# Kernel optimization log

Measured on AMD Instinct MI355X. Metric: run time of the kernel, lower is better.

The kernel has to match this reference:

```python
import jax, jax.numpy as jnp
import numpy as np

CS = [32, 32, 64, 128, 256, 256, 128, 96, 96]
NC = 19
N0, N1, N2, N3, N4 = 50000, 20000, 8000, 3200, 1300


def build_shapes():
    cs = CS
    def rb(ci, co):
        t = [(27, ci, co), (27, co, co)]
        if ci != co:
            t.append((ci, co))  # 1x1 shortcut conv
        return t
    s = [(27, 4, cs[0]), (27, cs[0], cs[0])]                       # stem
    s += [(8, cs[0], cs[0])] + rb(cs[0], cs[1]) + rb(cs[1], cs[1])  # stage1
    s += [(8, cs[1], cs[1])] + rb(cs[1], cs[2]) + rb(cs[2], cs[2])  # stage2
    s += [(8, cs[2], cs[2])] + rb(cs[2], cs[3]) + rb(cs[3], cs[3])  # stage3
    s += [(8, cs[3], cs[3])] + rb(cs[3], cs[4]) + rb(cs[4], cs[4])  # stage4
    s += [(8, cs[4], cs[5])] + rb(cs[5] + cs[3], cs[5]) + rb(cs[5], cs[5])  # up1
    s += [(8, cs[5], cs[6])] + rb(cs[6] + cs[2], cs[6]) + rb(cs[6], cs[6])  # up2
    s += [(8, cs[6], cs[7])] + rb(cs[7] + cs[1], cs[7]) + rb(cs[7], cs[7])  # up3
    s += [(8, cs[7], cs[8])] + rb(cs[8] + cs[0], cs[8]) + rb(cs[8], cs[8])  # up4
    s += [(cs[8], NC), (NC,), (cs[8], cs[8]), (cs[8],), (cs[8], 128), (128,)]
    return s

P_TOTAL = sum(int(np.prod(sh)) for sh in build_shapes())


def _bn(x):
    # train-mode BatchNorm, gamma=1 beta=0 (set by weight_initialization)
    return (x - x.mean(0)) * jax.lax.rsqrt(jnp.var(x, 0) + 1e-5)


def _spconv(x, nbr, W):
    # sparse conv as gather-GEMM-scatter over K kernel offsets.
    # x: [Nin, Cin], nbr: [Nout, K] row indices into x, W: [K, Cin, Cout]
    acc0 = jnp.zeros((nbr.shape[0], W.shape[-1]), x.dtype)
    def step(acc, kw):
        idx, Wk = kw
        return acc + x[idx] @ Wk, None
    acc, _ = jax.lax.scan(step, acc0, (nbr.T, W))
    return acc


def _spdeconv(x, parent, off, W):
    # transposed ks=2 stride=2 conv: each fine voxel has exactly one coarse
    # parent and one kernel-offset id. out[i] = x[parent[i]] @ W[off[i]]
    y = jnp.einsum('nc,kcd->nkd', x[parent], W)  # [Nf, 8, Cout]
    return jnp.take_along_axis(y, off[:, None, None], axis=1)[:, 0, :]


def _cbr(x, nbr, W):
    return jax.nn.relu(_bn(_spconv(x, nbr, W)))


def _resblock(x, nbr, take, ci, co):
    w1 = take(); w2 = take()
    h = _bn(_spconv(jax.nn.relu(_bn(_spconv(x, nbr, w1))), nbr, w2))
    s = x if ci == co else _bn(x @ take())
    return jax.nn.relu(h + s)


def _forward(x, nbr0, nbr1, nbr2, nbr3, nbr4, d1, d2, d3, d4,
             u1p, u1o, u2p, u2o, u3p, u3o, u4p, u4o, params):
    parts = []
    o = 0
    for sh in build_shapes():
        n = int(np.prod(sh))
        parts.append(params[o:o + n].reshape(sh))
        o += n
    it = iter(parts)
    take = lambda: next(it)
    cs = CS
    x0 = _cbr(x, nbr0, take()); x0 = _cbr(x0, nbr0, take())            # stem
    h = _cbr(x0, d1, take())
    h = _resblock(h, nbr1, take, cs[0], cs[1]); x1 = _resblock(h, nbr1, take, cs[1], cs[1])
    h = _cbr(x1, d2, take())
    h = _resblock(h, nbr2, take, cs[1], cs[2]); x2 = _resblock(h, nbr2, take, cs[2], cs[2])
    h = _cbr(x2, d3, take())
    h = _resblock(h, nbr3, take, cs[2], cs[3]); x3 = _resblock(h, nbr3, take, cs[3], cs[3])
    h = _cbr(x3, d4, take())
    h = _resblock(h, nbr4, take, cs[3], cs[4]); x4 = _resblock(h, nbr4, take, cs[4], cs[4])
    y = jax.nn.relu(_bn(_spdeconv(x4, u1p, u1o, take())))
    y = jnp.concatenate([y, x3], 1)
    y = _resblock(y, nbr3, take, cs[5] + cs[3], cs[5]); y = _resblock(y, nbr3, take, cs[5], cs[5])
    y = jax.nn.relu(_bn(_spdeconv(y, u2p, u2o, take())))
    y = jnp.concatenate([y, x2], 1)
    y = _resblock(y, nbr2, take, cs[6] + cs[2], cs[6]); y = _resblock(y, nbr2, take, cs[6], cs[6])
    y = jax.nn.relu(_bn(_spdeconv(y, u3p, u3o, take())))
    y = jnp.concatenate([y, x1], 1)
    y = _resblock(y, nbr1, take, cs[7] + cs[1], cs[7]); y = _resblock(y, nbr1, take, cs[7], cs[7])
    y = jax.nn.relu(_bn(_spdeconv(y, u4p, u4o, take())))
    y = jnp.concatenate([y, x0], 1)
    y = _resblock(y, nbr0, take, cs[8] + cs[0], cs[8]); y = _resblock(y, nbr0, take, cs[8], cs[8])
    wc = take(); bc = take(); w1 = take(); b1 = take(); w2 = take(); b2 = take()
    out = y @ wc + bc                             # classifier logits [N0, NC]
    feat = jax.nn.relu(y @ w1 + b1) @ w2 + b2     # projection head [N0, 128]
    return out, feat


def setup_inputs() -> dict:
    key = jax.random.key(0)
    ks = jax.random.split(key, 20)
    ri = lambda k, shape, hi: jax.random.randint(k, shape, 0, hi, dtype=jnp.int32)
    return {
        'x': jax.random.normal(ks[0], (N0, 4), jnp.float32),
        'nbr0': ri(ks[1], (N0, 27), N0), 'nbr1': ri(ks[2], (N1, 27), N1),
        'nbr2': ri(ks[3], (N2, 27), N2), 'nbr3': ri(ks[4], (N3, 27), N3),
        'nbr4': ri(ks[5], (N4, 27), N4),
        'd1': ri(ks[6], (N1, 8), N0), 'd2': ri(ks[7], (N2, 8), N1),
        'd3': ri(ks[8], (N3, 8), N2), 'd4': ri(ks[9], (N4, 8), N3),
        'u1p': ri(ks[10], (N3,), N4), 'u1o': ri(ks[11], (N3,), 8),
        'u2p': ri(ks[12], (N2,), N3), 'u2o': ri(ks[13], (N2,), 8),
        'u3p': ri(ks[14], (N1,), N2), 'u3o': ri(ks[15], (N1,), 8),
        'u4p': ri(ks[16], (N0,), N1), 'u4o': ri(ks[17], (N0,), 8),
        'params': jax.random.normal(ks[18], (P_TOTAL,), jnp.float32) * 0.05,
    }


def reference(x, nbr0, nbr1, nbr2, nbr3, nbr4, d1, d2, d3, d4,
              u1p, u1o, u2p, u2o, u3p, u3o, u4p, u4o, params):
    return _forward(x, nbr0, nbr1, nbr2, nbr3, nbr4, d1, d2, d3, d4,
                    u1p, u1o, u2p, u2o, u3p, u3o, u4p, u4o, params)
```

## Files before the change

kernel.cpp:

```cpp
#include <hip/hip_runtime.h>
#include <hip/hip_bf16.h>
#include <stdint.h>

typedef __hip_bfloat16 hbf;
typedef unsigned short u16;
typedef __attribute__((ext_vector_type(8))) short bfrag;
typedef _Float16 __attribute__((ext_vector_type(8))) hfrag;
typedef __attribute__((ext_vector_type(4))) float f4;

#define NP0 50000
#define NP1 20000
#define NP2 8000
#define NP3 3200
#define NP4 1300

static inline int cdiv(int a, int b) { return (a + b - 1) / b; }

static __device__ __forceinline__ float u2f(u16 u) { return __uint_as_float(((unsigned)u) << 16); }
static __device__ __forceinline__ u16 f2u(float f) {
  hbf h = __float2bfloat16(f);
  u16 r; __builtin_memcpy(&r, &h, 2); return r;
}
static __device__ __forceinline__ u16 f2h(float f) {
  _Float16 h = (_Float16)f;
  u16 r; __builtin_memcpy(&r, &h, 2); return r;
}
static __device__ __forceinline__ float h2f(u16 u) {
  _Float16 h; __builtin_memcpy(&h, &u, 2); return (float)h;
}
static __device__ __forceinline__ float pload(const void* P, int isbf, size_t i) {
  return isbf ? u2f(((const u16*)P)[i]) : ((const float*)P)[i];
}


struct PrepD {
  long cpre, src, dst;
  int K, CI, CO, CB32, NT16, hf;
};

__global__ void k_sniff(const void* __restrict__ xraw, int* __restrict__ flagp) {
  __shared__ float smax[256];
  const u16* u = (const u16*)xraw;
  float m = 0.f;
  for (int i = threadIdx.x; i < 2048; i += 256) {
    float v = u2f(u[2 * i]);
    if (isnan(v) || isinf(v)) m = 1e30f; else m = fmaxf(m, fabsf(v));
  }
  smax[threadIdx.x] = m;
  __syncthreads();
  for (int s = 128; s > 0; s >>= 1) {
    if (threadIdx.x < s) smax[threadIdx.x] = fmaxf(smax[threadIdx.x], smax[threadIdx.x + s]);
    __syncthreads();
  }
  if (threadIdx.x == 0) *flagp = (smax[0] < 1e4f) ? 1 : 0;
}

__global__ __launch_bounds__(256) void k_prep_all(
    const void* __restrict__ P, const int* __restrict__ flagp, u16* __restrict__ W,
    const PrepD* __restrict__ T, int NL, long totalC, long totalE)
{
  int f = *flagp;
  int L = 0;
  for (long c = (long)blockIdx.x * 256 + threadIdx.x; c < totalC; c += (long)gridDim.x * 256) {
    while (L + 1 < NL && c >= T[L + 1].cpre) ++L;
    PrepD d = T[L];
    long lc = c - d.cpre;
    int lane = (int)(lc & 63); long t = lc >> 6;
    int nt = (int)(t % d.NT16); t /= d.NT16;
    int cb = (int)(t % d.CB32); int k = (int)(t / d.CB32);
    int co = nt * 16 + (lane & 15);
    int cib = cb * 32 + (lane >> 4) * 8;
    u16 hi[8], lo[8];
#pragma unroll
    for (int j = 0; j < 8; ++j) {
      int ci = cib + j; float v = 0.f;
      if (ci < d.CI && co < d.CO) v = pload(P, f, d.src + ((size_t)k * d.CI + ci) * d.CO + co);
      if (d.hf) { u16 h = f2h(v); hi[j] = h; lo[j] = f2h(v - h2f(h)); }
      else      { u16 h = f2u(v); hi[j] = h; lo[j] = f2u(v - u2f(h)); }
    }
    *(bfrag*)(W + d.dst + lc * 8) = *(const bfrag*)hi;
    *(bfrag*)(W + totalE + d.dst + lc * 8) = *(const bfrag*)lo;
  }
}

__global__ __launch_bounds__(256) void k_prep_frag(
    const void* __restrict__ P, const int* __restrict__ flagp, u16* __restrict__ W,
    long src, long halfel, int hf, int K, int CI, int CO, int CB32, int NT16)
{
  int f = *flagp;
  long total = (long)K * CB32 * NT16 * 64;
  for (long c = (long)blockIdx.x * 256 + threadIdx.x; c < total; c += (long)gridDim.x * 256) {
    int lane = (int)(c & 63); long t = c >> 6;
    int nt = (int)(t % NT16); t /= NT16;
    int cb = (int)(t % CB32); int k = (int)(t / CB32);
    int co = nt * 16 + (lane & 15);
    int cib = cb * 32 + (lane >> 4) * 8;
    u16 hi[8], lo[8];
#pragma unroll
    for (int j = 0; j < 8; ++j) {
      int ci = cib + j; float v = 0.f;
      if (ci < CI && co < CO) v = pload(P, f, src + ((size_t)k * CI + ci) * CO + co);
      if (hf) { u16 h = f2h(v); hi[j] = h; lo[j] = f2h(v - h2f(h)); }
      else    { u16 h = f2u(v); hi[j] = h; lo[j] = f2u(v - u2f(h)); }
    }
    *(bfrag*)(W + c * 8) = *(const bfrag*)hi;
    *(bfrag*)(W + halfel + c * 8) = *(const bfrag*)lo;
  }
}

__global__ void k_prep_bias(const void* __restrict__ P, const int* __restrict__ flagp,
                            float* __restrict__ B, long src, int n)
{
  int f = *flagp;
  int i = blockIdx.x * 256 + threadIdx.x;
  if (i < n) B[i] = pload(P, f, src + i);
}

__global__ void k_pad(const void* __restrict__ xraw, const int* __restrict__ flagp,
                      float* __restrict__ Xp, int N)
{
  int f = *flagp; int total = N * 32;
  for (int i = blockIdx.x * 256 + threadIdx.x; i < total; i += gridDim.x * 256) {
    int n = i >> 5, cc = i & 31;
    Xp[i] = (cc < 4) ? pload(xraw, f, (size_t)n * 4 + cc) : 0.f;
  }
}

template<int NT>
__global__ __launch_bounds__(256) void k_conv_mfma(
    const void* __restrict__ Xv, const int* __restrict__ nbr,
    const u16* __restrict__ Wp, long halfel, float* __restrict__ Y,
    const float* __restrict__ bias, int relu, const int* __restrict__ flagp,
    int ahalf, int N, int K, int CB32, int NT16, int CO, int XS, int tlen, int atomic)
{
  const int f = *flagp;
  const int lane = threadIdx.x & 63;
  const int wv = threadIdx.x >> 6;
  const int rowbase = blockIdx.x * 128 + wv * 32;
  const int ntb = blockIdx.y * NT;
  const int ml = lane & 15;
  const int quad = lane >> 4;
  const int ktot = K * CB32;
  const int t0 = blockIdx.z * tlen;
  const int t1 = (t0 + tlen < ktot) ? (t0 + tlen) : ktot;
  if (t0 >= t1) return;

  f4 acc[2][NT];
#pragma unroll
  for (int i = 0; i < 2; ++i)
#pragma unroll
    for (int j = 0; j < NT; ++j) acc[i][j] = (f4)(0.f);

  int k = t0 / CB32;
  int cb = t0 - k * CB32;
  int idx[2];
  bool fresh = true;

  if (ahalf) {
    const u16* X = (const u16*)Xv;
    if (f) {
      for (int t = t0; t < t1; ++t) {
        if (fresh) {
#pragma unroll
          for (int mt = 0; mt < 2; ++mt) {
            int r = rowbase + mt * 16 + ml;
            idx[mt] = (r < N) ? (nbr ? nbr[(size_t)r * K + k] : r) : 0;
          }
          fresh = false;
        }
        const u16* WH = Wp + (size_t)t * NT16 * 512;
        hfrag bh[NT];
#pragma unroll
        for (int nt = 0; nt < NT; ++nt)
          bh[nt] = *(const hfrag*)(WH + ((size_t)(ntb + nt) * 64 + lane) * 8);
        hfrag a[2];
#pragma unroll
        for (int mt = 0; mt < 2; ++mt)
          a[mt] = *(const hfrag*)(X + (size_t)idx[mt] * XS + cb * 32 + quad * 8);
#pragma unroll
        for (int mt = 0; mt < 2; ++mt)
#pragma unroll
          for (int nt = 0; nt < NT; ++nt)
            acc[mt][nt] = __builtin_amdgcn_mfma_f32_16x16x32_f16(a[mt], bh[nt], acc[mt][nt], 0, 0, 0);
        if (++cb == CB32) { cb = 0; ++k; fresh = true; }
      }
    } else {
      for (int t = t0; t < t1; ++t) {
        if (fresh) {
#pragma unroll
          for (int mt = 0; mt < 2; ++mt) {
            int r = rowbase + mt * 16 + ml;
            idx[mt] = (r < N) ? (nbr ? nbr[(size_t)r * K + k] : r) : 0;
          }
          fresh = false;
        }
        const u16* WH = Wp + (size_t)t * NT16 * 512;
        const u16* WL = WH + halfel;
        hfrag bh[NT], bl[NT];
#pragma unroll
        for (int nt = 0; nt < NT; ++nt) {
          size_t o = ((size_t)(ntb + nt) * 64 + lane) * 8;
          bh[nt] = *(const hfrag*)(WH + o);
          bl[nt] = *(const hfrag*)(WL + o);
        }
        hfrag a[2];
#pragma unroll
        for (int mt = 0; mt < 2; ++mt)
          a[mt] = *(const hfrag*)(X + (size_t)idx[mt] * XS + cb * 32 + quad * 8);
#pragma unroll
        for (int mt = 0; mt < 2; ++mt)
#pragma unroll
          for (int nt = 0; nt < NT; ++nt) {
            acc[mt][nt] = __builtin_amdgcn_mfma_f32_16x16x32_f16(a[mt], bl[nt], acc[mt][nt], 0, 0, 0);
            acc[mt][nt] = __builtin_amdgcn_mfma_f32_16x16x32_f16(a[mt], bh[nt], acc[mt][nt], 0, 0, 0);
          }
        if (++cb == CB32) { cb = 0; ++k; fresh = true; }
      }
    }
  } else {
    const float* X = (const float*)Xv;
    if (f) {
      for (int t = t0; t < t1; ++t) {
        if (fresh) {
#pragma unroll
          for (int mt = 0; mt < 2; ++mt) {
            int r = rowbase + mt * 16 + ml;
            idx[mt] = (r < N) ? (nbr ? nbr[(size_t)r * K + k] : r) : 0;
          }
          fresh = false;
        }
        const u16* WH = Wp + (size_t)t * NT16 * 512;
        bfrag bh[NT];
#pragma unroll
        for (int nt = 0; nt < NT; ++nt)
          bh[nt] = *(const bfrag*)(WH + ((size_t)(ntb + nt) * 64 + lane) * 8);
        bfrag ahi[2], alo[2];
#pragma unroll
        for (int mt = 0; mt < 2; ++mt) {
          const float* ap = X + (size_t)idx[mt] * XS + cb * 32 + quad * 8;
          float4 q0 = *(const float4*)ap;
          float4 q1 = *(const float4*)(ap + 4);
          float av[8] = {q0.x, q0.y, q0.z, q0.w, q1.x, q1.y, q1.z, q1.w};
          u16 hi8[8], lo8[8];
#pragma unroll
          for (int j = 0; j < 8; ++j) {
            u16 hh = f2u(av[j]);
            hi8[j] = hh;
            lo8[j] = f2u(av[j] - u2f(hh));
          }
          __builtin_memcpy(&ahi[mt], hi8, 16);
          __builtin_memcpy(&alo[mt], lo8, 16);
        }
#pragma unroll
        for (int mt = 0; mt < 2; ++mt)
#pragma unroll
          for (int nt = 0; nt < NT; ++nt) {
            acc[mt][nt] = __builtin_amdgcn_mfma_f32_16x16x32_bf16(alo[mt], bh[nt], acc[mt][nt], 0, 0, 0);
            acc[mt][nt] = __builtin_amdgcn_mfma_f32_16x16x32_bf16(ahi[mt], bh[nt], acc[mt][nt], 0, 0, 0);
          }
        if (++cb == CB32) { cb = 0; ++k; fresh = true; }
      }
    } else {
      for (int t = t0; t < t1; ++t) {
        if (fresh) {
#pragma unroll
          for (int mt = 0; mt < 2; ++mt) {
            int r = rowbase + mt * 16 + ml;
            idx[mt] = (r < N) ? (nbr ? nbr[(size_t)r * K + k] : r) : 0;
          }
          fresh = false;
        }
        const u16* WH = Wp + (size_t)t * NT16 * 512;
        const u16* WL = WH + halfel;
        bfrag bh[NT], bl[NT];
#pragma unroll
        for (int nt = 0; nt < NT; ++nt) {
          size_t o = ((size_t)(ntb + nt) * 64 + lane) * 8;
          bh[nt] = *(const bfrag*)(WH + o);
          bl[nt] = *(const bfrag*)(WL + o);
        }
        bfrag ahi[2], alo[2];
#pragma unroll
        for (int mt = 0; mt < 2; ++mt) {
          const float* ap = X + (size_t)idx[mt] * XS + cb * 32 + quad * 8;
          float4 q0 = *(const float4*)ap;
          float4 q1 = *(const float4*)(ap + 4);
          float av[8] = {q0.x, q0.y, q0.z, q0.w, q1.x, q1.y, q1.z, q1.w};
          u16 hi8[8], lo8[8];
#pragma unroll
          for (int j = 0; j < 8; ++j) {
            u16 hh = f2u(av[j]);
            hi8[j] = hh;
            lo8[j] = f2u(av[j] - u2f(hh));
          }
          __builtin_memcpy(&ahi[mt], hi8, 16);
          __builtin_memcpy(&alo[mt], lo8, 16);
        }
#pragma unroll
        for (int mt = 0; mt < 2; ++mt)
#pragma unroll
          for (int nt = 0; nt < NT; ++nt) {
            acc[mt][nt] = __builtin_amdgcn_mfma_f32_16x16x32_bf16(alo[mt], bh[nt], acc[mt][nt], 0, 0, 0);
            acc[mt][nt] = __builtin_amdgcn_mfma_f32_16x16x32_bf16(ahi[mt], bl[nt], acc[mt][nt], 0, 0, 0);
            acc[mt][nt] = __builtin_amdgcn_mfma_f32_16x16x32_bf16(ahi[mt], bh[nt], acc[mt][nt], 0, 0, 0);
          }
        if (++cb == CB32) { cb = 0; ++k; fresh = true; }
      }
    }
  }

#pragma unroll
  for (int mt = 0; mt < 2; ++mt) {
#pragma unroll
    for (int nt = 0; nt < NT; ++nt) {
      int col = (ntb + nt) * 16 + ml;
      if (col >= CO) continue;
      float bvv = bias ? bias[col] : 0.f;
#pragma unroll
      for (int reg = 0; reg < 4; ++reg) {
        int row = rowbase + mt * 16 + quad * 4 + reg;
        if (row < N) {
          if (atomic) {
            atomicAdd(&Y[(size_t)row * CO + col], acc[mt][nt][reg]);
          } else {
            float v = acc[mt][nt][reg] + bvv;
            if (relu) v = fmaxf(v, 0.f);
            Y[(size_t)row * CO + col] = v;
          }
        }
      }
    }
  }
}

__global__ void k_bias_relu(float* __restrict__ Y, const float* __restrict__ bias,
                            u16* __restrict__ d16, int relu, int total, int CO)
{
  int stride = gridDim.x * 256;
  for (int i = blockIdx.x * 256 + threadIdx.x; i < total; i += stride) {
    int c = i % CO;
    float v = Y[i] + (bias ? bias[c] : 0.f);
    if (relu) v = fmaxf(v, 0.f);
    Y[i] = v;
    if (d16) d16[i] = f2h(v);
  }
}

static void launch_conv(hipStream_t s, int bx, const void* X, const int* nbr,
                        const u16* W, long halfel, float* Y, const float* bias, int relu,
                        const int* flagp, int ahalf, int N, int K, int CB32, int NT16, int CO, int XS,
                        u16* d16)
{
  int NT = (NT16 % 6 == 0) ? 6 : ((NT16 % 4 == 0) ? 4 : 2);
  int ny = NT16 / NT;
  int ktot = K * CB32;
  long blocks = (long)bx * ny;
  int ZS = 1;
  if (ktot > 1) {
    ZS = (int)((1024 + blocks - 1) / blocks);
    if (ZS > ktot) ZS = ktot;
    if (ZS < 1) ZS = 1;
  }
  int tlen = cdiv(ktot, ZS);
  ZS = cdiv(ktot, tlen);
  int atomic = (ZS > 1) ? 1 : 0;
  if (atomic) hipMemsetAsync(Y, 0, (size_t)N * CO * 4, s);
  dim3 g(bx, ny, ZS);
  if (NT == 6)      k_conv_mfma<6><<<g, 256, 0, s>>>(X, nbr, W, halfel, Y, bias, relu, flagp, ahalf, N, K, CB32, NT16, CO, XS, tlen, atomic);
  else if (NT == 4) k_conv_mfma<4><<<g, 256, 0, s>>>(X, nbr, W, halfel, Y, bias, relu, flagp, ahalf, N, K, CB32, NT16, CO, XS, tlen, atomic);
  else              k_conv_mfma<2><<<g, 256, 0, s>>>(X, nbr, W, halfel, Y, bias, relu, flagp, ahalf, N, K, CB32, NT16, CO, XS, tlen, atomic);
  if ((atomic && (bias || relu)) || d16) {
    int total = N * CO;
    int nb = cdiv(total, 1024); if (nb > 1024) nb = 1024; if (nb < 1) nb = 1;
    k_bias_relu<<<nb, 256, 0, s>>>(Y, atomic ? bias : nullptr, d16, atomic ? relu : 0, total, CO);
  }
}

__global__ __launch_bounds__(256) void k_deconv(
    const void* __restrict__ Xv, const int* __restrict__ par, const int* __restrict__ off,
    const void* __restrict__ P, long wofs, const int* __restrict__ flagp,
    float* __restrict__ Y, int xmode, int N, int CI, int CO)
{
  int f = *flagp;
  int lane = threadIdx.x & 63, wv = threadIdx.x >> 6;
  int n = blockIdx.y * 4 + wv; if (n >= N) return;
  int co = blockIdx.x * 64 + lane; if (co >= CO) return;
  size_t wbase = wofs + (size_t)off[n] * CI * CO + co;
  float acc = 0.f;
  if (xmode) {
    const u16* xr = (const u16*)Xv + (size_t)par[n] * CI;
    for (int ci = 0; ci < CI; ci += 4) {
      ushort4 xv = *(const ushort4*)(xr + ci);
      acc += h2f(xv.x) * pload(P, f, wbase + (size_t)ci * CO);
      acc += h2f(xv.y) * pload(P, f, wbase + (size_t)(ci + 1) * CO);
      acc += h2f(xv.z) * pload(P, f, wbase + (size_t)(ci + 2) * CO);
      acc += h2f(xv.w) * pload(P, f, wbase + (size_t)(ci + 3) * CO);
    }
  } else {
    const float* xr = (const float*)Xv + (size_t)par[n] * CI;
    for (int ci = 0; ci < CI; ci += 4) {
      float4 xv = *(const float4*)(xr + ci);
      acc += xv.x * pload(P, f, wbase + (size_t)ci * CO);
      acc += xv.y * pload(P, f, wbase + (size_t)(ci + 1) * CO);
      acc += xv.z * pload(P, f, wbase + (size_t)(ci + 2) * CO);
      acc += xv.w * pload(P, f, wbase + (size_t)(ci + 3) * CO);
    }
  }
  Y[(size_t)n * CO + co] = acc;
}

__global__ __launch_bounds__(256) void k_bn_stats(
    const float* __restrict__ X, float* __restrict__ st, int total, int C)
{
  __shared__ float ssum[384], ssq[384];
  for (int c = threadIdx.x; c < C; c += 256) { ssum[c] = 0.f; ssq[c] = 0.f; }
  __syncthreads();
  int gid = blockIdx.x * 256 + threadIdx.x;
  int total4 = total >> 2;
  int stride = gridDim.x * 256;
  int c0 = (gid * 4) % C;
  float s0 = 0.f, s1 = 0.f, s2 = 0.f, s3 = 0.f;
  float q0 = 0.f, q1 = 0.f, q2 = 0.f, q3 = 0.f;
  for (int i = gid; i < total4; i += stride) {
    float4 v = ((const float4*)X)[i];
    s0 += v.x; q0 += v.x * v.x;
    s1 += v.y; q1 += v.y * v.y;
    s2 += v.z; q2 += v.z * v.z;
    s3 += v.w; q3 += v.w * v.w;
  }
  atomicAdd(&ssum[c0], s0);     atomicAdd(&ssq[c0], q0);
  atomicAdd(&ssum[c0 + 1], s1); atomicAdd(&ssq[c0 + 1], q1);
  atomicAdd(&ssum[c0 + 2], s2); atomicAdd(&ssq[c0 + 2], q2);
  atomicAdd(&ssum[c0 + 3], s3); atomicAdd(&ssq[c0 + 3], q3);
  __syncthreads();
  for (int c = threadIdx.x; c < C; c += 256) {
    atomicAdd(&st[c], ssum[c]); atomicAdd(&st[384 + c], ssq[c]);
  }
}

__global__ __launch_bounds__(256) void k_bn_apply(
    const float* __restrict__ X, const float* __restrict__ st,
    const void* __restrict__ addp, int addmode,
    void* __restrict__ Yo, int outmode, int relu, int total, int C, float invN)
{
  __shared__ float mean[384], rsig[384];
  for (int c = threadIdx.x; c < C; c += 256) {
    float mm = st[c] * invN;
    float vv = st[384 + c] * invN - mm * mm;
    mean[c] = mm; rsig[c] = rsqrtf(vv + 1e-5f);
  }
  __syncthreads();
  int gid = blockIdx.x * 256 + threadIdx.x;
  int total4 = total >> 2;
  int stride = gridDim.x * 256;
  int c0 = (gid * 4) % C;
  float m0 = mean[c0], m1 = mean[c0 + 1], m2 = mean[c0 + 2], m3 = mean[c0 + 3];
  float r0 = rsig[c0], r1 = rsig[c0 + 1], r2 = rsig[c0 + 2], r3 = rsig[c0 + 3];
  for (int i = gid; i < total4; i += stride) {
    float4 v = ((const float4*)X)[i];
    float w0 = (v.x - m0) * r0, w1 = (v.y - m1) * r1;
    float w2 = (v.z - m2) * r2, w3 = (v.w - m3) * r3;
    if (addmode == 1) {
      float4 a = ((const float4*)addp)[i];
      w0 += a.x; w1 += a.y; w2 += a.z; w3 += a.w;
    } else if (addmode == 2) {
      ushort4 ah = *(const ushort4*)((const u16*)addp + (size_t)i * 4);
      w0 += h2f(ah.x); w1 += h2f(ah.y); w2 += h2f(ah.z); w3 += h2f(ah.w);
    }
    if (relu) {
      w0 = fmaxf(w0, 0.f); w1 = fmaxf(w1, 0.f);
      w2 = fmaxf(w2, 0.f); w3 = fmaxf(w3, 0.f);
    }
    if (outmode == 0) {
      float4 o; o.x = w0; o.y = w1; o.z = w2; o.w = w3;
      ((float4*)Yo)[i] = o;
    } else {
      ushort4 hh; hh.x = f2h(w0); hh.y = f2h(w1); hh.z = f2h(w2); hh.w = f2h(w3);
      *(ushort4*)((u16*)Yo + (size_t)i * 4) = hh;
    }
  }
}

__global__ void k_copycols(const void* __restrict__ Sv, u16* __restrict__ D,
                           int smode, int N, int Cs, int Cd, int off)
{
  int csq = Cs >> 2;
  int total4 = N * csq;
  int stride = gridDim.x * 256;
  for (int i = blockIdx.x * 256 + threadIdx.x; i < total4; i += stride) {
    int n = i / csq, cc = (i - n * csq) * 4;
    ushort4 hh;
    if (smode == 0) {
      float4 v = ((const float4*)Sv)[i];
      hh.x = f2h(v.x); hh.y = f2h(v.y); hh.z = f2h(v.z); hh.w = f2h(v.w);
    } else {
      hh = *(const ushort4*)((const u16*)Sv + (size_t)i * 4);
    }
    *(ushort4*)(D + (size_t)n * Cd + off + cc) = hh;
  }
}

__global__ void k_store_dyn(const float* __restrict__ S, void* __restrict__ D,
                            const int* __restrict__ flagp, size_t eofs, int n)
{
  int f = *flagp;
  int n4 = n >> 2;
  int stride = gridDim.x * 256;
  for (int i = blockIdx.x * 256 + threadIdx.x; i < n4; i += stride) {
    float4 v = ((const float4*)S)[i];
    if (f) {
      ushort4 u;
      u.x = f2u(v.x); u.y = f2u(v.y); u.z = f2u(v.z); u.w = f2u(v.w);
      *(ushort4*)((u16*)D + eofs + (size_t)i * 4) = u;
    } else {
      *(float4*)((float*)D + eofs + (size_t)i * 4) = v;
    }
  }
}

static int build_table(PrepD* T, long* totalC, long* totalE) {
  int n = 0; long po = 0, ce = 0, cc = 0;
  auto W = [&](int K, int CI, int CO, int hf) {
    int CB = cdiv(CI, 32), NTx = cdiv(CO, 16);
    long ch = (long)K * CB * NTx * 64;
    T[n].cpre = cc; T[n].src = po; T[n].dst = ce;
    T[n].K = K; T[n].CI = CI; T[n].CO = CO; T[n].CB32 = CB; T[n].NT16 = NTx; T[n].hf = hf;
    ++n; cc += ch; ce += ch * 8; po += (long)K * CI * CO;
  };
  auto SKIP = [&](long e) { po += e; };
  W(27, 4, 32, 0); W(27, 32, 32, 0);
  W(8, 32, 32, 0); W(27, 32, 32, 0); W(27, 32, 32, 0); W(27, 32, 32, 0); W(27, 32, 32, 0);
  W(8, 32, 32, 0); W(27, 32, 64, 0); W(27, 64, 64, 0); W(1, 32, 64, 0); W(27, 64, 64, 0); W(27, 64, 64, 0);
  W(8, 64, 64, 0); W(27, 64, 128, 0); W(27, 128, 128, 0); W(1, 64, 128, 0); W(27, 128, 128, 0); W(27, 128, 128, 0);
  W(8, 128, 128, 0); W(27, 128, 256, 0); W(27, 256, 256, 0); W(1, 128, 256, 0); W(27, 256, 256, 0); W(27, 256, 256, 0);
  SKIP(8L * 256 * 256);
  W(27, 384, 256, 1); W(27, 256, 256, 1); W(1, 384, 256, 1); W(27, 256, 256, 1); W(27, 256, 256, 1);
  SKIP(8L * 256 * 128);
  W(27, 192, 128, 1); W(27, 128, 128, 1); W(1, 192, 128, 1); W(27, 128, 128, 1); W(27, 128, 128, 1);
  SKIP(8L * 128 * 96);
  W(27, 128, 96, 1); W(27, 96, 96, 1); W(1, 128, 96, 1); W(27, 96, 96, 1); W(27, 96, 96, 1);
  SKIP(8L * 96 * 96);
  W(27, 128, 96, 1); W(27, 96, 96, 1); W(1, 128, 96, 1); W(27, 96, 96, 1); W(27, 96, 96, 1);
  W(1, 96, 19, 1); SKIP(19); W(1, 96, 96, 1); SKIP(96); W(1, 96, 128, 1); SKIP(128);
  *totalC = cc; *totalE = ce;
  return n;
}

extern "C" void kernel_launch(void* const* d_in, const int* in_sizes, int n_in,
                              void* d_out, int out_size, void* d_ws, size_t ws_size,
                              hipStream_t stream)
{
  const void* xraw = d_in[0];
  const int* nbr0 = (const int*)d_in[1];
  const int* nbr1 = (const int*)d_in[2];
  const int* nbr2 = (const int*)d_in[3];
  const int* nbr3 = (const int*)d_in[4];
  const int* nbr4 = (const int*)d_in[5];
  const int* d1 = (const int*)d_in[6];
  const int* d2 = (const int*)d_in[7];
  const int* d3 = (const int*)d_in[8];
  const int* d4 = (const int*)d_in[9];
  const int* u1p = (const int*)d_in[10]; const int* u1o = (const int*)d_in[11];
  const int* u2p = (const int*)d_in[12]; const int* u2o = (const int*)d_in[13];
  const int* u3p = (const int*)d_in[14]; const int* u3o = (const int*)d_in[15];
  const int* u4p = (const int*)d_in[16]; const int* u4o = (const int*)d_in[17];
  const void* params = d_in[18];
  (void)in_sizes; (void)n_in;

  static PrepD h_table[64];
  long totalC = 0, totalE = 0;
  int NL = build_table(h_table, &totalC, &totalE);

  char* base = (char*)d_ws; size_t off = 0;
  auto ab = [&](size_t bytes) -> void* { void* p = base + off; off += (bytes + 63) & ~(size_t)63; return p; };
  int* flagp = (int*)ab(64);
  float* st = (float*)ab((size_t)64 * 768 * 4);
  float* Bstf = (float*)ab((size_t)512 * 4);
  float* x0 = (float*)ab((size_t)NP0 * 32 * 4);
  float* x1 = (float*)ab((size_t)NP1 * 32 * 4);
  float* x2 = (float*)ab((size_t)NP2 * 64 * 4);
  float* x3 = (float*)ab((size_t)NP3 * 128 * 4);
  float* x4 = (float*)ab((size_t)NP4 * 256 * 4);
  float* U  = (float*)ab((size_t)NP0 * 96 * 4);
  float* A  = (float*)ab((size_t)NP0 * 96 * 4);
  float* B  = (float*)ab((size_t)NP0 * 128 * 4);
  float* Xp = B;

  size_t wall_bytes = (size_t)totalE * 4;
  size_t rem = (ws_size > off) ? (ws_size - off) : 0;
  bool bigprep = rem >= wall_bytes + 8192;
  u16* Wall = nullptr; PrepD* d_table = nullptr; u16* Wst = nullptr;
  if (bigprep) {
    Wall = (u16*)ab(wall_bytes);
    d_table = (PrepD*)ab(4096);
  } else {
    Wst = (u16*)ab((size_t)5400000 * 2);
  }
  if (off > ws_size) { hipMemsetAsync(d_out, 0, (size_t)out_size * 2, stream); return; }

  long po = 0;
  int bnc = 0;
  int wli = 0;

  auto prepF = [&](int hf, int K, int CI, int CO, int CB32, int NT16) -> long {
    long chunks = (long)K * CB32 * NT16 * 64;
    long halfel = chunks * 8;
    int nb = (int)((chunks + 255) / 256); if (nb > 4096) nb = 4096; if (nb < 1) nb = 1;
    k_prep_frag<<<nb, 256, 0, stream>>>(params, flagp, Wst, po, halfel, hf, K, CI, CO, CB32, NT16);
    po += (long)K * CI * CO;
    return halfel;
  };
  auto getW = [&](int hf, int K, int CI, int CO, int CB32, int NT16, const u16** Wp, long* he) {
    if (bigprep) {
      *Wp = Wall + h_table[wli].dst; *he = totalE;
      ++wli; po += (long)K * CI * CO;
    } else {
      *he = prepF(hf, K, CI, CO, CB32, NT16); *Wp = Wst;
    }
  };
  auto convop = [&](int hf, const void* X, const int* nb_, int K, int CI, int CO, float* Y, int N, int XS) {
    int CB32 = cdiv(CI, 32), NT16 = cdiv(CO, 16);
    const u16* Wp; long he;
    getW(hf, K, CI, CO, CB32, NT16, &Wp, &he);
    launch_conv(stream, cdiv(N, 128), X, nb_, Wp, he, Y, nullptr, 0, flagp, hf, N, K, CB32, NT16, CO, XS, nullptr);
  };
  auto linop = [&](int hf, const void* X, int CI, int CO, float* Y, int N, bool bias, int relu, u16* d16) {
    int CB32 = cdiv(CI, 32), NT16 = cdiv(CO, 16);
    const u16* Wp; long he;
    getW(hf, 1, CI, CO, CB32, NT16, &Wp, &he);
    const float* bp = nullptr;
    if (bias) {
      k_prep_bias<<<cdiv(CO, 256), 256, 0, stream>>>(params, flagp, Bstf, po, CO);
      po += CO; bp = Bstf;
    }
    launch_conv(stream, cdiv(N, 128), X, nullptr, Wp, he, Y, bp, relu, flagp, hf, N, 1, CB32, NT16, CO, CI, d16);
  };
  auto deconvop = [&](const void* X, int xmode, const int* par, const int* ofv, int CI, int CO, float* Y, int N) {
    long wofs = po; po += (long)8 * CI * CO;
    dim3 g(cdiv(CO, 64), cdiv(N, 4));
    k_deconv<<<g, 256, 0, stream>>>(X, par, ofv, params, wofs, flagp, Y, xmode, N, CI, CO);
  };
  auto bnop = [&](const float* X, int N, int C, const void* addp, int addmode, int relu,
                  void* out, int outmode) {
    float* slot = st + (size_t)(bnc++) * 768;
    int total = N * C;
    int total4 = total >> 2;
    int nb1 = cdiv(total4, 4096); if (nb1 > 504) nb1 = 504; if (nb1 < 3) nb1 = 3;
    nb1 = ((nb1 + 2) / 3) * 3;
    k_bn_stats<<<nb1, 256, 0, stream>>>(X, slot, total, C);
    int nb2 = cdiv(total4, 2048); if (nb2 > 510) nb2 = 510; if (nb2 < 3) nb2 = 3;
    nb2 = ((nb2 + 2) / 3) * 3;
    k_bn_apply<<<nb2, 256, 0, stream>>>(X, slot, addp, addmode, out ? out : (void*)X, outmode,
                                        relu, total, C, 1.0f / (float)N);
  };
  auto copyop = [&](const void* S, int smode, u16* D, int N, int Cs, int Cd, int o2) {
    int total4 = (N * Cs) >> 2;
    int nb3 = cdiv(total4, 1024); if (nb3 > 1024) nb3 = 1024; if (nb3 < 1) nb3 = 1;
    k_copycols<<<nb3, 256, 0, stream>>>(S, D, smode, N, Cs, Cd, o2);
  };
  auto storeop = [&](const float* S, size_t eo, int n) {
    int nb4 = cdiv(n >> 2, 1024); if (nb4 > 1024) nb4 = 1024; if (nb4 < 1) nb4 = 1;
    k_store_dyn<<<nb4, 256, 0, stream>>>(S, d_out, flagp, eo, n);
  };
  auto resblock = [&](const int* nb, int N, int CI, int CO,
                      float* H, float* t1, float* t2, float* OUT) {
    convop(0, H, nb, 27, CI, CO, t1, N, CI);
    bnop(t1, N, CO, nullptr, 0, 1, nullptr, 0);
    convop(0, t1, nb, 27, CO, CO, t2, N, CO);
    const float* S;
    if (CI == CO) S = H;
    else { linop(0, H, CI, CO, t1, N, false, 0, nullptr); bnop(t1, N, CO, nullptr, 0, 0, nullptr, 0); S = t1; }
    bnop(t2, N, CO, S, 1, 1, OUT, 0);
  };
  auto resblock16 = [&](const int* nb, int N, int CI, int CO,
                        u16* H16, float* t1, float* t2, u16* OUT16) {
    convop(1, H16, nb, 27, CI, CO, t1, N, CI);
    bnop(t1, N, CO, nullptr, 0, 1, (u16*)t2, 1);
    convop(1, (u16*)t2, nb, 27, CO, CO, t1, N, CO);
    if (CI == CO) {
      bnop(t1, N, CO, H16, 2, 1, OUT16, 1);
    } else {
      linop(1, H16, CI, CO, t2, N, false, 0, nullptr);
      bnop(t2, N, CO, nullptr, 0, 0, OUT16, 1);
      bnop(t1, N, CO, OUT16, 2, 1, OUT16, 1);
    }
  };

  k_sniff<<<1, 256, 0, stream>>>(xraw, flagp);
  if (bigprep) {
    hipMemcpyAsync(d_table, h_table, (size_t)NL * sizeof(PrepD), hipMemcpyHostToDevice, stream);
    int nbp = (int)((totalC + 255) / 256); if (nbp > 4096) nbp = 4096;
    k_prep_all<<<nbp, 256, 0, stream>>>(params, flagp, Wall, d_table, NL, totalC, totalE);
  }
  hipMemsetAsync(st, 0, (size_t)64 * 768 * 4, stream);
  k_pad<<<1024, 256, 0, stream>>>(xraw, flagp, Xp, NP0);

  convop(0, Xp, nbr0, 27, 4, 32, A, NP0, 32);  bnop(A, NP0, 32, nullptr, 0, 1, nullptr, 0);
  convop(0, A, nbr0, 27, 32, 32, x0, NP0, 32); bnop(x0, NP0, 32, nullptr, 0, 1, nullptr, 0);
  convop(0, x0, d1, 8, 32, 32, U, NP1, 32); bnop(U, NP1, 32, nullptr, 0, 1, nullptr, 0);
  resblock(nbr1, NP1, 32, 32, U, A, B, U);
  resblock(nbr1, NP1, 32, 32, U, A, B, x1);
  convop(0, x1, d2, 8, 32, 32, U, NP2, 32); bnop(U, NP2, 32, nullptr, 0, 1, nullptr, 0);
  resblock(nbr2, NP2, 32, 64, U, A, B, U);
  resblock(nbr2, NP2, 64, 64, U, A, B, x2);
  convop(0, x2, d3, 8, 64, 64, U, NP3, 64); bnop(U, NP3, 64, nullptr, 0, 1, nullptr, 0);
  resblock(nbr3, NP3, 64, 128, U, A, B, U);
  resblock(nbr3, NP3, 128, 128, U, A, B, x3);
  convop(0, x3, d4, 8, 128, 128, U, NP4, 128); bnop(U, NP4, 128, nullptr, 0, 1, nullptr, 0);
  resblock(nbr4, NP4, 128, 256, U, A, B, U);
  resblock(nbr4, NP4, 256, 256, U, A, B, x4);

  u16* U16 = (u16*)U; u16* B16 = (u16*)B; u16* A16 = (u16*)A;
  deconvop(x4, 0, u1p, u1o, 256, 256, A, NP3);
  bnop(A, NP3, 256, nullptr, 0, 1, U16, 1);
  copyop(U16, 1, B16, NP3, 256, 384, 0); copyop(x3, 0, B16, NP3, 128, 384, 256);
  resblock16(nbr3, NP3, 384, 256, B16, A, U, B16);
  resblock16(nbr3, NP3, 256, 256, B16, A, U, U16);
  deconvop(U16, 1, u2p, u2o, 256, 128, A, NP2);
  bnop(A, NP2, 128, nullptr, 0, 1, U16, 1);
  copyop(U16, 1, B16, NP2, 128, 192, 0); copyop(x2, 0, B16, NP2, 64, 192, 128);
  resblock16(nbr2, NP2, 192, 128, B16, A, U, B16);
  resblock16(nbr2, NP2, 128, 128, B16, A, U, U16);
  deconvop(U16, 1, u3p, u3o, 128, 96, A, NP1);
  bnop(A, NP1, 96, nullptr, 0, 1, U16, 1);
  copyop(U16, 1, B16, NP1, 96, 128, 0); copyop(x1, 0, B16, NP1, 32, 128, 96);
  resblock16(nbr1, NP1, 128, 96, B16, A, U, B16);
  resblock16(nbr1, NP1, 96, 96, B16, A, U, U16);
  deconvop(U16, 1, u4p, u4o, 96, 96, A, NP0);
  bnop(A, NP0, 96, nullptr, 0, 1, U16, 1);
  copyop(U16, 1, B16, NP0, 96, 128, 0); copyop(x0, 0, B16, NP0, 32, 128, 96);
  resblock16(nbr0, NP0, 128, 96, B16, A, U, B16);
  resblock16(nbr0, NP0, 96, 96, B16, A, U, U16);
  float* x0f = (float*)x0;
  linop(1, U16, 96, 19, x0f, NP0, true, 0, nullptr);
  linop(1, U16, 96, 96, B, NP0, true, 1, A16);
  linop(1, A16, 96, 128, B, NP0, true, 0, nullptr);
  storeop(x0f, 0, NP0 * 19);
  storeop(B, (size_t)NP0 * 19, NP0 * 128);
}
```

Before: 4.015 ms.

## Run transposed convs through the MFMA gather-conv kernel with a zero-row index table

Replaces the scalar per-output deconv kernel with the existing MFMA gather-GEMM conv path. A small kernel builds an 8-entry neighbor table per fine voxel that points at the parent for its own offset and at an appended zero row for the other seven, and the deconv weights are now prepacked like the other conv weights. This swaps a scalar loop that reads weights uncoalesced for matrix-core GEMMs, at the cost of eight times more multiply work (seven of every eight products are against zeros) plus extra memset and index-building launches.

After: 3.886 ms. 3.2% less time.

```diff
diff --git a/kernel.cpp b/kernel.cpp
--- a/kernel.cpp
+++ b/kernel.cpp
@@ -126,6 +126,17 @@
   }
 }
 
+__global__ void k_mk_didx(const int* __restrict__ par, const int* __restrict__ off,
+                          int* __restrict__ idx, int N, int ZR)
+{
+  int stride = gridDim.x * 256;
+  for (int i = blockIdx.x * 256 + threadIdx.x; i < N; i += stride) {
+    int p = par[i], o = off[i];
+#pragma unroll
+    for (int k = 0; k < 8; ++k) idx[(size_t)i * 8 + k] = (k == o) ? p : ZR;
+  }
+}
+
 template<int NT>
 __global__ __launch_bounds__(256) void k_conv_mfma(
     const void* __restrict__ Xv, const int* __restrict__ nbr,
@@ -374,39 +385,6 @@
     int nb = cdiv(total, 1024); if (nb > 1024) nb = 1024; if (nb < 1) nb = 1;
     k_bias_relu<<<nb, 256, 0, s>>>(Y, atomic ? bias : nullptr, d16, atomic ? relu : 0, total, CO);
   }
-}
-
-__global__ __launch_bounds__(256) void k_deconv(
-    const void* __restrict__ Xv, const int* __restrict__ par, const int* __restrict__ off,
-    const void* __restrict__ P, long wofs, const int* __restrict__ flagp,
-    float* __restrict__ Y, int xmode, int N, int CI, int CO)
-{
-  int f = *flagp;
-  int lane = threadIdx.x & 63, wv = threadIdx.x >> 6;
-  int n = blockIdx.y * 4 + wv; if (n >= N) return;
-  int co = blockIdx.x * 64 + lane; if (co >= CO) return;
-  size_t wbase = wofs + (size_t)off[n] * CI * CO + co;
-  float acc = 0.f;
-  if (xmode) {
-    const u16* xr = (const u16*)Xv + (size_t)par[n] * CI;
-    for (int ci = 0; ci < CI; ci += 4) {
-      ushort4 xv = *(const ushort4*)(xr + ci);
-      acc += h2f(xv.x) * pload(P, f, wbase + (size_t)ci * CO);
-      acc += h2f(xv.y) * pload(P, f, wbase + (size_t)(ci + 1) * CO);
-      acc += h2f(xv.z) * pload(P, f, wbase + (size_t)(ci + 2) * CO);
-      acc += h2f(xv.w) * pload(P, f, wbase + (size_t)(ci + 3) * CO);
-    }
-  } else {
-    const float* xr = (const float*)Xv + (size_t)par[n] * CI;
-    for (int ci = 0; ci < CI; ci += 4) {
-      float4 xv = *(const float4*)(xr + ci);
-      acc += xv.x * pload(P, f, wbase + (size_t)ci * CO);
-      acc += xv.y * pload(P, f, wbase + (size_t)(ci + 1) * CO);
-      acc += xv.z * pload(P, f, wbase + (size_t)(ci + 2) * CO);
-      acc += xv.w * pload(P, f, wbase + (size_t)(ci + 3) * CO);
-    }
-  }
-  Y[(size_t)n * CO + co] = acc;
 }
 
 __global__ __launch_bounds__(256) void k_bn_stats(
@@ -533,13 +511,13 @@
   W(8, 32, 32, 0); W(27, 32, 64, 0); W(27, 64, 64, 0); W(1, 32, 64, 0); W(27, 64, 64, 0); W(27, 64, 64, 0);
   W(8, 64, 64, 0); W(27, 64, 128, 0); W(27, 128, 128, 0); W(1, 64, 128, 0); W(27, 128, 128, 0); W(27, 128, 128, 0);
   W(8, 128, 128, 0); W(27, 128, 256, 0); W(27, 256, 256, 0); W(1, 128, 256, 0); W(27, 256, 256, 0); W(27, 256, 256, 0);
-  SKIP(8L * 256 * 256);
+  W(8, 256, 256, 0);
   W(27, 384, 256, 1); W(27, 256, 256, 1); W(1, 384, 256, 1); W(27, 256, 256, 1); W(27, 256, 256, 1);
-  SKIP(8L * 256 * 128);
+  W(8, 256, 128, 1);
   W(27, 192, 128, 1); W(27, 128, 128, 1); W(1, 192, 128, 1); W(27, 128, 128, 1); W(27, 128, 128, 1);
-  SKIP(8L * 128 * 96);
+  W(8, 128, 96, 1);
   W(27, 128, 96, 1); W(27, 96, 96, 1); W(1, 128, 96, 1); W(27, 96, 96, 1); W(27, 96, 96, 1);
-  SKIP(8L * 96 * 96);
+  W(8, 96, 96, 1);
   W(27, 128, 96, 1); W(27, 96, 96, 1); W(1, 128, 96, 1); W(27, 96, 96, 1); W(27, 96, 96, 1);
   W(1, 96, 19, 1); SKIP(19); W(1, 96, 96, 1); SKIP(96); W(1, 96, 128, 1); SKIP(128);
   *totalC = cc; *totalE = ce;
@@ -576,11 +554,12 @@
   int* flagp = (int*)ab(64);
   float* st = (float*)ab((size_t)64 * 768 * 4);
   float* Bstf = (float*)ab((size_t)512 * 4);
+  int* didx = (int*)ab((size_t)NP0 * 8 * 4);
   float* x0 = (float*)ab((size_t)NP0 * 32 * 4);
   float* x1 = (float*)ab((size_t)NP1 * 32 * 4);
   float* x2 = (float*)ab((size_t)NP2 * 64 * 4);
   float* x3 = (float*)ab((size_t)NP3 * 128 * 4);
-  float* x4 = (float*)ab((size_t)NP4 * 256 * 4);
+  float* x4 = (float*)ab((size_t)(NP4 + 1) * 256 * 4);
   float* U  = (float*)ab((size_t)NP0 * 96 * 4);
   float* A  = (float*)ab((size_t)NP0 * 96 * 4);
   float* B  = (float*)ab((size_t)NP0 * 128 * 4);
@@ -635,10 +614,13 @@
     }
     launch_conv(stream, cdiv(N, 128), X, nullptr, Wp, he, Y, bp, relu, flagp, hf, N, 1, CB32, NT16, CO, CI, d16);
   };
-  auto deconvop = [&](const void* X, int xmode, const int* par, const int* ofv, int CI, int CO, float* Y, int N) {
-    long wofs = po; po += (long)8 * CI * CO;
-    dim3 g(cdiv(CO, 64), cdiv(N, 4));
-    k_deconv<<<g, 256, 0, stream>>>(X, par, ofv, params, wofs, flagp, Y, xmode, N, CI, CO);
+  auto deconvop = [&](int hf, const void* X, int Ns, const int* par, const int* ofv,
+                      int CI, int CO, float* Y, int N) {
+    if (hf) hipMemsetAsync((u16*)X + (size_t)Ns * CI, 0, (size_t)CI * 2, stream);
+    else    hipMemsetAsync((float*)X + (size_t)Ns * CI, 0, (size_t)CI * 4, stream);
+    int nbl = cdiv(N, 256); if (nbl > 1024) nbl = 1024; if (nbl < 1) nbl = 1;
+    k_mk_didx<<<nbl, 256, 0, stream>>>(par, ofv, didx, N, Ns);
+    convop(hf, X, didx, 8, CI, CO, Y, N, CI);
   };
   auto bnop = [&](const float* X, int N, int C, const void* addp, int addmode, int relu,
                   void* out, int outmode) {
@@ -711,22 +693,22 @@
   resblock(nbr4, NP4, 256, 256, U, A, B, x4);
 
   u16* U16 = (u16*)U; u16* B16 = (u16*)B; u16* A16 = (u16*)A;
-  deconvop(x4, 0, u1p, u1o, 256, 256, A, NP3);
+  deconvop(0, x4, NP4, u1p, u1o, 256, 256, A, NP3);
   bnop(A, NP3, 256, nullptr, 0, 1, U16, 1);
   copyop(U16, 1, B16, NP3, 256, 384, 0); copyop(x3, 0, B16, NP3, 128, 384, 256);
   resblock16(nbr3, NP3, 384, 256, B16, A, U, B16);
   resblock16(nbr3, NP3, 256, 256, B16, A, U, U16);
-  deconvop(U16, 1, u2p, u2o, 256, 128, A, NP2);
+  deconvop(1, U16, NP3, u2p, u2o, 256, 128, A, NP2);
   bnop(A, NP2, 128, nullptr, 0, 1, U16, 1);
   copyop(U16, 1, B16, NP2, 128, 192, 0); copyop(x2, 0, B16, NP2, 64, 192, 128);
   resblock16(nbr2, NP2, 192, 128, B16, A, U, B16);
   resblock16(nbr2, NP2, 128, 128, B16, A, U, U16);
-  deconvop(U16, 1, u3p, u3o, 128, 96, A, NP1);
+  deconvop(1, U16, NP2, u3p, u3o, 128, 96, A, NP1);
   bnop(A, NP1, 96, nullptr, 0, 1, U16, 1);
   copyop(U16, 1, B16, NP1, 96, 128, 0); copyop(x1, 0, B16, NP1, 32, 128, 96);
   resblock16(nbr1, NP1, 128, 96, B16, A, U, B16);
   resblock16(nbr1, NP1, 96, 96, B16, A, U, U16);
-  deconvop(U16, 1, u4p, u4o, 96, 96, A, NP0);
+  deconvop(1, U16, NP1, u4p, u4o, 96, 96, A, NP0);
   bnop(A, NP0, 96, nullptr, 0, 1, U16, 1);
   copyop(U16, 1, B16, NP0, 96, 128, 0); copyop(x0, 0, B16, NP0, 32, 128, 96);
   resblock16(nbr0, NP0, 128, 96, B16, A, U, B16);
```
